# Kernel optimization log

Measured on AMD Instinct MI355X. Metric: run time of the kernel, lower is better.

## Reference

```python
import jax, jax.numpy as jnp
import numpy as np

N, T, D_MODEL, H, DK = 4, 4096, 1024, 16, 64


def setup_inputs() -> dict:
    key = jax.random.key(0)
    ks = jax.random.split(key, 16)
    randn = lambda k, sh: jax.random.normal(k, sh, dtype=jnp.float32)
    # linear weights stored (in, out) so y = x @ W + b (math-equivalent to torch Linear)
    scale = 1.0 / np.sqrt(D_MODEL)
    return {
        "x_k": randn(ks[0], (N, T, D_MODEL)),
        "x_v": randn(ks[1], (N, T, D_MODEL)),
        "x_q": randn(ks[2], (N, T, D_MODEL)),
        "mask": jnp.ones((N, T), dtype=jnp.int32),
        "Wk": randn(ks[3], (D_MODEL, H * DK)) * scale,
        "bk": randn(ks[4], (H * DK,)) * 0.02,
        "Wv": randn(ks[5], (D_MODEL, H * DK)) * scale,
        "bv": randn(ks[6], (H * DK,)) * 0.02,
        "Wq": randn(ks[7], (D_MODEL, H * DK)) * scale,
        "bq": randn(ks[8], (H * DK,)) * 0.02,
        "alpha_w": randn(ks[9], (DK,)),
        "beta_w": randn(ks[10], (DK,)),
        "Wr": randn(ks[11], (DK, DK)) * (1.0 / np.sqrt(DK)),
        "br": randn(ks[12], (DK,)) * 0.02,
        "Wfc": randn(ks[13], (H * DK, D_MODEL)) * scale,
        "bfc": randn(ks[14], (D_MODEL,)) * 0.02,
    }


def _split_heads(x):  # (n, t, h*d) -> (n, h, t, d)
    n, t, _ = x.shape
    return x.reshape(n, t, H, DK).transpose(0, 2, 1, 3)


def reference(x_k, x_v, x_q, mask, Wk, bk, Wv, bv, Wq, bq,
              alpha_w, beta_w, Wr, br, Wfc, bfc):
    scale = DK ** (-0.5)
    k = _split_heads(x_k @ Wk + bk)  # (n, h, t, d)
    v = _split_heads(x_v @ Wv + bv)
    q = _split_heads(x_q @ Wq + bq)

    m = (mask == 0)[:, None, :]  # (n, 1, t) True where masked
    neg_inf = jnp.finfo(q.dtype).min

    # alpha pooling over queries -> global query (n, h, d)
    alpha = jnp.einsum('nhtd,d->nht', q, alpha_w) * scale
    alpha = jnp.where(m, neg_inf, alpha)
    alpha = jax.nn.softmax(alpha, axis=-1)
    global_query = jnp.einsum('nht,nhtd->nhd', alpha, q)

    # p = broadcast(global_query) * k, then beta pooling -> global key
    p = global_query[:, :, None, :] * k  # (n, h, t, d)
    beta = jnp.einsum('nhtd,d->nht', p, beta_w) * scale
    beta = jnp.where(m, neg_inf, beta)
    beta = jax.nn.softmax(beta, axis=-1)
    global_key = jnp.einsum('nht,nhtd->nhd', beta, p)

    u = global_key[:, :, None, :] * v  # (n, h, t, d)
    u_r = u @ Wr + br
    A = u_r + q  # (n, h, t, d)
    A = A.transpose(0, 2, 1, 3).reshape(N, T, H * DK)
    return A @ Wfc + bfc
```

## Files before the change

kernel.cpp:

```cpp
#include <hip/hip_runtime.h>

typedef __bf16 bf16x8 __attribute__((ext_vector_type(8)));
typedef float f32x4 __attribute__((ext_vector_type(4)));
typedef unsigned int u32x4 __attribute__((ext_vector_type(4)));
typedef unsigned short u16x4 __attribute__((ext_vector_type(4)));
typedef unsigned short u16x8 __attribute__((ext_vector_type(8)));

#define SEQ_T 4096
#define DMODEL 1024
#define HEADS 16
#define DKH 64
#define MTOK 16384

#define AS1 __attribute__((address_space(1)))
#define AS3 __attribute__((address_space(3)))

__device__ __forceinline__ unsigned short f2bf(float f) {
  unsigned u = __builtin_bit_cast(unsigned int, f);
  u += 0x7FFFu + ((u >> 16) & 1u);
  return (unsigned short)(u >> 16);
}
__device__ __forceinline__ float bf2f(unsigned short h) {
  unsigned u = ((unsigned)h) << 16;
  return __builtin_bit_cast(float, u);
}
__device__ __forceinline__ void gload16(const unsigned short* g, unsigned short* l) {
  __builtin_amdgcn_global_load_lds((const AS1 unsigned int*)(g),
                                   (AS3 unsigned int*)(l), 16, 0, 0);
}

__global__ void __launch_bounds__(256) k_cvt(const float* __restrict__ x,
                                             unsigned short* __restrict__ y,
                                             long long nelem) {
  long long i = ((long long)blockIdx.x * 256 + threadIdx.x) * 8;
  if (i >= nelem) return;
  u16x8 o;
#pragma unroll
  for (int j = 0; j < 8; ++j) o[j] = f2bf(x[i + j]);
  *(u16x8*)(y + i) = o;
}

__global__ void __launch_bounds__(256) k_wtrans(const float* __restrict__ W,
                                                unsigned short* __restrict__ Wt,
                                                int K, int N) {
  __shared__ float tile[32][33];
  int bn = blockIdx.x * 32, bk = blockIdx.y * 32;
  int tx = threadIdx.x, ty = threadIdx.y;
#pragma unroll
  for (int j = 0; j < 32; j += 8)
    tile[ty + j][tx] = W[(size_t)(bk + ty + j) * N + bn + tx];
  __syncthreads();
#pragma unroll
  for (int j = 0; j < 32; j += 8)
    Wt[(size_t)(bn + ty + j) * K + bk + tx] = f2bf(tile[tx][ty + j]);
}

#define BM 128
#define BN 128
#define BK 32

template <int OBF, int SCORE>
__global__ void __launch_bounds__(256, 2)
k_gemm(const unsigned short* __restrict__ A, const unsigned short* __restrict__ Bt,
       const float* __restrict__ bias, void* __restrict__ C,
       const int* __restrict__ mask, const float* __restrict__ swt,
       float* __restrict__ sbuf, int M, int N, int K) {
  __shared__ unsigned short As[BM * BK];
  __shared__ unsigned short Bs[BN * BK];
  const int tid = threadIdx.x;
  const int lane = tid & 63, wid = tid >> 6;
  const int wr = wid >> 1, wc = wid & 1;
  const int bnb = blockIdx.x;
  const int bm = blockIdx.y * BM, bn = bnb * BN;
  const int l15 = lane & 15, l4 = lane >> 4;

  f32x4 acc[4][4];
#pragma unroll
  for (int i = 0; i < 4; ++i)
#pragma unroll
    for (int j = 0; j < 4; ++j)
#pragma unroll
      for (int e = 0; e < 4; ++e) acc[i][j][e] = 0.f;

  const int srow = wid * 32 + (lane >> 2);
  const int scol = (lane & 3) * 8;
  const unsigned short* Ag = A + (size_t)(bm + srow) * K + scol;
  const unsigned short* Bg = Bt + (size_t)(bn + srow) * K + scol;
  unsigned short* Al = As + wid * 32 * BK;
  unsigned short* Bl = Bs + wid * 32 * BK;

  for (int kt = 0; kt < K; kt += BK) {
    __syncthreads();
    gload16(Ag + kt, Al);
    gload16(Ag + kt + 16 * K, Al + 16 * BK);
    gload16(Bg + kt, Bl);
    gload16(Bg + kt + 16 * K, Bl + 16 * BK);
    __syncthreads();
    bf16x8 af[4], bfr[4];
#pragma unroll
    for (int m = 0; m < 4; ++m)
      af[m] = *(const bf16x8*)(As + (wr * 64 + m * 16 + l15) * BK + l4 * 8);
#pragma unroll
    for (int n = 0; n < 4; ++n)
      bfr[n] = *(const bf16x8*)(Bs + (wc * 64 + n * 16 + l15) * BK + l4 * 8);
#pragma unroll
    for (int m = 0; m < 4; ++m)
#pragma unroll
      for (int n = 0; n < 4; ++n)
        acc[m][n] = __builtin_amdgcn_mfma_f32_16x16x32_bf16(af[m], bfr[n],
                                                            acc[m][n], 0, 0, 0);
  }

  const int crow = bm + wr * 64 + l4 * 4;
  const int ccol = bn + wc * 64 + l15;

  float pacc[4][4];
  const float* wrow = nullptr;
  if (SCORE == 1) wrow = swt;
  if (SCORE == 2) wrow = swt + ((size_t)((bm >> 12) * HEADS + bnb * 2 + wc)) * DKH;
  if (SCORE) {
#pragma unroll
    for (int m = 0; m < 4; ++m)
#pragma unroll
      for (int e = 0; e < 4; ++e) pacc[m][e] = 0.f;
  }

#pragma unroll
  for (int m = 0; m < 4; ++m)
#pragma unroll
    for (int n = 0; n < 4; ++n) {
      int c = ccol + n * 16;
      float bj = bias[c];
      float wg = SCORE ? wrow[n * 16 + l15] : 0.f;
#pragma unroll
      for (int e = 0; e < 4; ++e) {
        int r = crow + m * 16 + e;
        float v = acc[m][n][e] + bj;
        if (SCORE) pacc[m][e] += v * wg;
        if (OBF)
          ((unsigned short*)C)[(size_t)r * N + c] = f2bf(v);
        else
          ((float*)C)[(size_t)r * N + c] = v;
      }
    }

  if (SCORE) {
#pragma unroll
    for (int m = 0; m < 4; ++m)
#pragma unroll
      for (int e = 0; e < 4; ++e) {
        float p = pacc[m][e];
        p += __shfl_xor(p, 1);
        p += __shfl_xor(p, 2);
        p += __shfl_xor(p, 4);
        p += __shfl_xor(p, 8);
        if (l15 == 0) {
          int r = crow + m * 16 + e;
          int t = r & (SEQ_T - 1), n = r >> 12;
          float sc = p * 0.125f;
          if (mask[n * SEQ_T + t] == 0) sc = -3.0e38f;
          sbuf[((size_t)n * HEADS + bnb * 2 + wc) * SEQ_T + t] = sc;
        }
      }
  }
}

__global__ void __launch_bounds__(256) k_stat1(const float* __restrict__ s,
                                               float* __restrict__ pmax,
                                               float* __restrict__ psum) {
  __shared__ float red[4];
  const int b = blockIdx.x, tid = threadIdx.x, lane = tid & 63, wid = tid >> 6;
  float v = s[(size_t)b * 256 + tid];
  float m = v;
#pragma unroll
  for (int o = 1; o < 64; o <<= 1) m = fmaxf(m, __shfl_xor(m, o));
  if (lane == 0) red[wid] = m;
  __syncthreads();
  m = fmaxf(fmaxf(red[0], red[1]), fmaxf(red[2], red[3]));
  __syncthreads();
  float e = __expf(v - m);
#pragma unroll
  for (int o = 1; o < 64; o <<= 1) e += __shfl_xor(e, o);
  if (lane == 0) red[wid] = e;
  __syncthreads();
  if (tid == 0) {
    pmax[b] = m;
    psum[b] = red[0] + red[1] + red[2] + red[3];
  }
}

__global__ void __launch_bounds__(64) k_stat2(const float* __restrict__ pmax,
                                              const float* __restrict__ psum,
                                              float* __restrict__ smx,
                                              float* __restrict__ sinv) {
  const int b = blockIdx.x, lane = threadIdx.x;
  float pm = -3.4e38f, ps = 0.f;
  if (lane < 16) {
    pm = pmax[b * 16 + lane];
    ps = psum[b * 16 + lane];
  }
  float gm = pm;
#pragma unroll
  for (int o = 1; o < 16; o <<= 1) gm = fmaxf(gm, __shfl_xor(gm, o));
  float sc = ps * __expf(pm - gm);
#pragma unroll
  for (int o = 1; o < 16; o <<= 1) sc += __shfl_xor(sc, o);
  if (lane == 0) {
    smx[b] = gm;
    sinv[b] = 1.f / sc;
  }
}

__global__ void __launch_bounds__(256) k_wsum(const unsigned short* __restrict__ X,
                                              const float* __restrict__ s,
                                              const float* __restrict__ mxv,
                                              const float* __restrict__ invv,
                                              float* __restrict__ pbuf) {
  __shared__ float part[16][64];
  const int nh = blockIdx.x >> 4, chunk = blockIdx.x & 15;
  const int n = nh >> 4, h = nh & 15;
  const int tid = threadIdx.x, lane = tid & 63, wid = tid >> 6;
  const int tsub = lane >> 4, dl = lane & 15;
  const float mx = mxv[nh], inv = invv[nh];
  const float* sb = s + (size_t)nh * SEQ_T + chunk * 256;
  const size_t base = ((size_t)n * SEQ_T + chunk * 256) * DMODEL + h * DKH + dl * 4;
  f32x4 acc = {0.f, 0.f, 0.f, 0.f};
  for (int t = wid * 4 + tsub; t < 256; t += 16) {
    float w = __expf(sb[t] - mx) * inv;
    u16x4 xv = *(const u16x4*)(X + base + (size_t)t * DMODEL);
    acc[0] += w * bf2f(xv[0]);
    acc[1] += w * bf2f(xv[1]);
    acc[2] += w * bf2f(xv[2]);
    acc[3] += w * bf2f(xv[3]);
  }
  int g = wid * 4 + tsub;
#pragma unroll
  for (int e = 0; e < 4; ++e) part[g][dl * 4 + e] = acc[e];
  __syncthreads();
  if (tid < 64) {
    float v = 0.f;
#pragma unroll
    for (int gg = 0; gg < 16; ++gg) v += part[gg][tid];
    pbuf[(size_t)blockIdx.x * 64 + tid] = v;
  }
}

template <int MODE>
__global__ void __launch_bounds__(64) k_fin(const float* __restrict__ pbuf,
                                            const float* __restrict__ gq,
                                            const float* __restrict__ bw,
                                            float* __restrict__ out,
                                            float* __restrict__ wv) {
  const int nh = blockIdx.x, d = threadIdx.x;
  float v = 0.f;
#pragma unroll
  for (int c = 0; c < 16; ++c) v += pbuf[((size_t)nh * 16 + c) * 64 + d];
  if (MODE == 1) v *= gq[(size_t)nh * 64 + d];
  out[(size_t)nh * 64 + d] = v;
  if (MODE == 0) wv[(size_t)nh * 64 + d] = v * bw[d];
}

__global__ void __launch_bounds__(256) k_wrg(const float* __restrict__ gk,
                                             const float* __restrict__ Wr,
                                             unsigned short* __restrict__ WrgT) {
  const int nh = blockIdx.x, tid = threadIdx.x;
#pragma unroll
  for (int i = 0; i < 16; ++i) {
    int idx = i * 256 + tid;
    int d = idx >> 6, dd = idx & 63;
    WrgT[(size_t)nh * 4096 + idx] = f2bf(gk[nh * 64 + dd] * Wr[dd * 64 + d]);
  }
}

#define ABM 128
#define VLD 72
__global__ void __launch_bounds__(256) k_abuild2(const unsigned short* __restrict__ v,
                                                 const unsigned short* __restrict__ qbf,
                                                 const unsigned short* __restrict__ WrgT,
                                                 const float* __restrict__ br,
                                                 unsigned short* __restrict__ A) {
  __shared__ unsigned short Vs[ABM * VLD];
  __shared__ unsigned short Ws[DKH * VLD];
  const int tid = threadIdx.x, lane = tid & 63, wid = tid >> 6;
  const int nh = blockIdx.y;
  const int n = nh >> 4, h = nh & 15;
  const size_t nt0 = (size_t)n * SEQ_T + (size_t)blockIdx.x * ABM;
  const size_t vbase = nt0 * DMODEL + (size_t)h * DKH;
#pragma unroll
  for (int p = 0; p < 4; ++p) {
    int idx = p * 256 + tid;
    int row = idx >> 3, c = idx & 7;
    *(u32x4*)(Vs + row * VLD + c * 8) =
        *(const u32x4*)(v + vbase + (size_t)row * DMODEL + c * 8);
  }
#pragma unroll
  for (int p = 0; p < 2; ++p) {
    int idx = p * 256 + tid;
    int row = idx >> 3, c = idx & 7;
    *(u32x4*)(Ws + row * VLD + c * 8) =
        *(const u32x4*)(WrgT + (size_t)nh * 4096 + row * 64 + c * 8);
  }
  __syncthreads();
  const int l15 = lane & 15, l4 = lane >> 4;
  f32x4 acc[2][4];
#pragma unroll
  for (int m = 0; m < 2; ++m)
#pragma unroll
    for (int nf = 0; nf < 4; ++nf)
#pragma unroll
      for (int e = 0; e < 4; ++e) acc[m][nf][e] = 0.f;
#pragma unroll
  for (int ks = 0; ks < 2; ++ks) {
    bf16x8 af[2], bfr[4];
#pragma unroll
    for (int m = 0; m < 2; ++m)
      af[m] = *(const bf16x8*)(Vs + (wid * 32 + m * 16 + l15) * VLD + l4 * 8 + ks * 32);
#pragma unroll
    for (int nf = 0; nf < 4; ++nf)
      bfr[nf] = *(const bf16x8*)(Ws + (nf * 16 + l15) * VLD + l4 * 8 + ks * 32);
#pragma unroll
    for (int m = 0; m < 2; ++m)
#pragma unroll
      for (int nf = 0; nf < 4; ++nf)
        acc[m][nf] = __builtin_amdgcn_mfma_f32_16x16x32_bf16(af[m], bfr[nf],
                                                             acc[m][nf], 0, 0, 0);
  }
#pragma unroll
  for (int m = 0; m < 2; ++m)
#pragma unroll
    for (int nf = 0; nf < 4; ++nf) {
      int d = nf * 16 + l15;
      float bj = br[d];
#pragma unroll
      for (int e = 0; e < 4; ++e) {
        int r = wid * 32 + m * 16 + l4 * 4 + e;
        size_t off = vbase + (size_t)r * DMODEL + d;
        float val = acc[m][nf][e] + bj + bf2f(qbf[off]);
        A[off] = f2bf(val);
      }
    }
}

extern "C" void kernel_launch(void* const* d_in, const int* in_sizes, int n_in,
                              void* d_out, int out_size, void* d_ws, size_t ws_size,
                              hipStream_t stream) {
  const float* x_k = (const float*)d_in[0];
  const float* x_v = (const float*)d_in[1];
  const float* x_q = (const float*)d_in[2];
  const int* mask = (const int*)d_in[3];
  const float* Wk = (const float*)d_in[4];
  const float* bk = (const float*)d_in[5];
  const float* Wv = (const float*)d_in[6];
  const float* bv = (const float*)d_in[7];
  const float* Wq = (const float*)d_in[8];
  const float* bq = (const float*)d_in[9];
  const float* alpha_w = (const float*)d_in[10];
  const float* beta_w = (const float*)d_in[11];
  const float* Wr = (const float*)d_in[12];
  const float* br = (const float*)d_in[13];
  const float* Wfc = (const float*)d_in[14];
  const float* bfc = (const float*)d_in[15];

  unsigned short* qbf = (unsigned short*)d_out;

  char* ws = (char*)d_ws;
  const size_t SZ_XBF = (size_t)MTOK * DMODEL * 2;
  unsigned short* kbf = (unsigned short*)(ws);
  unsigned short* vbf = (unsigned short*)(ws + SZ_XBF);
  unsigned short* xst = (unsigned short*)(ws + 2 * SZ_XBF);
  unsigned short* WkT = (unsigned short*)(ws + 3 * SZ_XBF);
  unsigned short* WvT = WkT + (size_t)DMODEL * DMODEL;
  unsigned short* WqT = WvT + (size_t)DMODEL * DMODEL;
  unsigned short* WfT = WqT + (size_t)DMODEL * DMODEL;
  unsigned short* WrgT = WfT + (size_t)DMODEL * DMODEL;
  float* gq = (float*)(WrgT + (size_t)64 * 4096);
  float* gk = gq + 4096;
  float* wvb = gk + 4096;
  float* sbuf = wvb + 4096;
  float* pbuf = sbuf + (size_t)64 * SEQ_T;
  float* pmax = pbuf + 1024 * 64;
  float* psum = pmax + 1024;
  float* smx = psum + 1024;
  float* sinv = smx + 64;

  dim3 tb(32, 8);
  dim3 tg(DMODEL / 32, DMODEL / 32);
  k_wtrans<<<tg, tb, 0, stream>>>(Wq, WqT, DMODEL, DMODEL);
  k_wtrans<<<tg, tb, 0, stream>>>(Wk, WkT, DMODEL, DMODEL);
  k_wtrans<<<tg, tb, 0, stream>>>(Wv, WvT, DMODEL, DMODEL);
  k_wtrans<<<tg, tb, 0, stream>>>(Wfc, WfT, DMODEL, DMODEL);

  long long nx = (long long)MTOK * DMODEL;
  int cvtg = (int)(nx / 8 / 256);
  dim3 ggrid(DMODEL / BN, MTOK / BM);

  k_cvt<<<cvtg, 256, 0, stream>>>(x_q, xst, nx);
  k_gemm<1, 1><<<ggrid, 256, 0, stream>>>(xst, WqT, bq, (void*)qbf, mask, alpha_w,
                                          sbuf, MTOK, DMODEL, DMODEL);
  k_stat1<<<1024, 256, 0, stream>>>(sbuf, pmax, psum);
  k_stat2<<<64, 64, 0, stream>>>(pmax, psum, smx, sinv);
  k_wsum<<<1024, 256, 0, stream>>>(qbf, sbuf, smx, sinv, pbuf);
  k_fin<0><<<64, 64, 0, stream>>>(pbuf, nullptr, beta_w, gq, wvb);

  k_cvt<<<cvtg, 256, 0, stream>>>(x_k, xst, nx);
  k_gemm<1, 2><<<ggrid, 256, 0, stream>>>(xst, WkT, bk, (void*)kbf, mask, wvb,
                                          sbuf, MTOK, DMODEL, DMODEL);
  k_stat1<<<1024, 256, 0, stream>>>(sbuf, pmax, psum);
  k_stat2<<<64, 64, 0, stream>>>(pmax, psum, smx, sinv);
  k_wsum<<<1024, 256, 0, stream>>>(kbf, sbuf, smx, sinv, pbuf);
  k_fin<1><<<64, 64, 0, stream>>>(pbuf, gq, nullptr, gk, nullptr);

  k_cvt<<<cvtg, 256, 0, stream>>>(x_v, xst, nx);
  k_gemm<1, 0><<<ggrid, 256, 0, stream>>>(xst, WvT, bv, (void*)vbf, nullptr, nullptr,
                                          nullptr, MTOK, DMODEL, DMODEL);

  k_wrg<<<64, 256, 0, stream>>>(gk, Wr, WrgT);
  dim3 agrid(SEQ_T / ABM, 64);
  k_abuild2<<<agrid, 256, 0, stream>>>(vbf, qbf, WrgT, br, xst);

  k_gemm<0, 0><<<ggrid, 256, 0, stream>>>(xst, WfT, bfc, d_out, nullptr, nullptr,
                                          nullptr, MTOK, DMODEL, DMODEL);
}
```

Before: 328.4 us.

## Eliminate K projection GEMM and fold Wr/global key into V weights

The full K projection GEMM is replaced by algebra. Beta scores are computed as x_k times a per-batch folded weight (Wk·(gq⊙beta_w)), giving a narrow 16-column GEMM. The global key is obtained by pooling raw x_k with the softmax weights and then projecting through Wk. The V projection, the Wr mixing and the q residual are fused into a single GEMM with per-batch combined weights (Wv·diag(gk)·Wr) and a combined bias, which removes the separate abuild pass and the kbf/vbf intermediates. In exchange it adds several small weight-prep kernels, an fp32 pooled pass over x_k, and per-batch weight matrices that change the rounding behaviour.

Measured after the change: 320.5 us. 1.02x faster.

```diff
diff --git a/kernel.cpp b/kernel.cpp
--- a/kernel.cpp
+++ b/kernel.cpp
@@ -59,12 +59,13 @@
 #define BN 128
 #define BK 32
 
-template <int OBF, int SCORE>
+template <int OBF, int SCORE, int FUSEA>
 __global__ void __launch_bounds__(256, 2)
 k_gemm(const unsigned short* __restrict__ A, const unsigned short* __restrict__ Bt,
        const float* __restrict__ bias, void* __restrict__ C,
        const int* __restrict__ mask, const float* __restrict__ swt,
-       float* __restrict__ sbuf, int M, int N, int K) {
+       float* __restrict__ sbuf, const unsigned short* __restrict__ qadd,
+       int M, int N, int K) {
   __shared__ unsigned short As[BM * BK];
   __shared__ unsigned short Bs[BN * BK];
   const int tid = threadIdx.x;
@@ -74,6 +75,9 @@
   const int bm = blockIdx.y * BM, bn = bnb * BN;
   const int l15 = lane & 15, l4 = lane >> 4;
 
+  const unsigned short* Btn = FUSEA ? Bt + ((size_t)(bm >> 12) << 20) : Bt;
+  const float* biasn = FUSEA ? bias + ((bm >> 12) << 10) : bias;
+
   f32x4 acc[4][4];
 #pragma unroll
   for (int i = 0; i < 4; ++i)
@@ -85,7 +89,7 @@
   const int srow = wid * 32 + (lane >> 2);
   const int scol = (lane & 3) * 8;
   const unsigned short* Ag = A + (size_t)(bm + srow) * K + scol;
-  const unsigned short* Bg = Bt + (size_t)(bn + srow) * K + scol;
+  const unsigned short* Bg = Btn + (size_t)(bn + srow) * K + scol;
   unsigned short* Al = As + wid * 32 * BK;
   unsigned short* Bl = Bs + wid * 32 * BK;
 
@@ -117,7 +121,6 @@
   float pacc[4][4];
   const float* wrow = nullptr;
   if (SCORE == 1) wrow = swt;
-  if (SCORE == 2) wrow = swt + ((size_t)((bm >> 12) * HEADS + bnb * 2 + wc)) * DKH;
   if (SCORE) {
 #pragma unroll
     for (int m = 0; m < 4; ++m)
@@ -130,12 +133,13 @@
 #pragma unroll
     for (int n = 0; n < 4; ++n) {
       int c = ccol + n * 16;
-      float bj = bias[c];
+      float bj = biasn[c];
       float wg = SCORE ? wrow[n * 16 + l15] : 0.f;
 #pragma unroll
       for (int e = 0; e < 4; ++e) {
         int r = crow + m * 16 + e;
         float v = acc[m][n][e] + bj;
+        if (FUSEA) v += bf2f(qadd[(size_t)r * N + c]);
         if (SCORE) pacc[m][e] += v * wg;
         if (OBF)
           ((unsigned short*)C)[(size_t)r * N + c] = f2bf(v);
@@ -245,9 +249,7 @@
   }
 }
 
-template <int MODE>
 __global__ void __launch_bounds__(64) k_fin(const float* __restrict__ pbuf,
-                                            const float* __restrict__ gq,
                                             const float* __restrict__ bw,
                                             float* __restrict__ out,
                                             float* __restrict__ wv) {
@@ -255,9 +257,167 @@
   float v = 0.f;
 #pragma unroll
   for (int c = 0; c < 16; ++c) v += pbuf[((size_t)nh * 16 + c) * 64 + d];
-  if (MODE == 1) v *= gq[(size_t)nh * 64 + d];
   out[(size_t)nh * 64 + d] = v;
-  if (MODE == 0) wv[(size_t)nh * 64 + d] = v * bw[d];
+  wv[(size_t)nh * 64 + d] = v * bw[d];
+}
+
+__global__ void __launch_bounds__(256) k_wks(const float* __restrict__ Wk,
+                                             const float* __restrict__ wv,
+                                             unsigned short* __restrict__ WksT) {
+  const int nh = blockIdx.x, tid = threadIdx.x;
+  const int n = nh >> 4, h = nh & 15;
+  __shared__ float wvs[64];
+  if (tid < 64) wvs[tid] = wv[(size_t)nh * 64 + tid];
+  __syncthreads();
+  int c0 = tid * 4;
+  u16x4 o;
+#pragma unroll
+  for (int i = 0; i < 4; ++i) {
+    int c = c0 + i;
+    const float* wr = Wk + (size_t)c * DMODEL + h * DKH;
+    float acc = 0.f;
+#pragma unroll
+    for (int dd = 0; dd < 64; dd += 4) {
+      f32x4 w4 = *(const f32x4*)(wr + dd);
+      acc += w4[0] * wvs[dd] + w4[1] * wvs[dd + 1] + w4[2] * wvs[dd + 2] +
+             w4[3] * wvs[dd + 3];
+    }
+    o[i] = f2bf(acc);
+  }
+  *(u16x4*)(WksT + (size_t)n * 16 * DMODEL + (size_t)h * DMODEL + c0) = o;
+}
+
+__global__ void __launch_bounds__(64) k_bks(const float* __restrict__ bk,
+                                            const float* __restrict__ wv,
+                                            float* __restrict__ bks) {
+  const int nh = blockIdx.x, dd = threadIdx.x;
+  const int h = nh & 15;
+  float p = bk[h * 64 + dd] * wv[(size_t)nh * 64 + dd];
+#pragma unroll
+  for (int o = 1; o < 64; o <<= 1) p += __shfl_xor(p, o);
+  if (dd == 0) bks[nh] = p;
+}
+
+__global__ void __launch_bounds__(128) k_score(const unsigned short* __restrict__ xk,
+                                               const unsigned short* __restrict__ WksT,
+                                               const float* __restrict__ bks,
+                                               const int* __restrict__ mask,
+                                               float* __restrict__ sbuf) {
+  __shared__ unsigned short Xs[64 * 32];
+  __shared__ unsigned short Ws[16 * 32];
+  const int tid = threadIdx.x, lane = tid & 63, wid = tid >> 6;
+  const int l15 = lane & 15, l4 = lane >> 4;
+  const int bm = blockIdx.x * 64;
+  const int n = bm >> 12;
+  const unsigned short* Wn = WksT + (size_t)n * 16 * DMODEL;
+
+  f32x4 acc[2];
+#pragma unroll
+  for (int m = 0; m < 2; ++m)
+#pragma unroll
+    for (int e = 0; e < 4; ++e) acc[m][e] = 0.f;
+
+  const int srow = lane >> 2, scol = (lane & 3) * 8;
+  for (int kt = 0; kt < DMODEL; kt += 32) {
+    __syncthreads();
+#pragma unroll
+    for (int j = 0; j < 2; ++j) {
+      int rb = wid * 32 + j * 16;
+      gload16(xk + (size_t)(bm + rb + srow) * DMODEL + kt + scol, Xs + rb * 32);
+    }
+    if (wid == 0) gload16(Wn + (size_t)srow * DMODEL + kt + scol, Ws);
+    __syncthreads();
+    bf16x8 bfr = *(const bf16x8*)(Ws + l15 * 32 + l4 * 8);
+#pragma unroll
+    for (int m = 0; m < 2; ++m) {
+      bf16x8 af = *(const bf16x8*)(Xs + (wid * 32 + m * 16 + l15) * 32 + l4 * 8);
+      acc[m] = __builtin_amdgcn_mfma_f32_16x16x32_bf16(af, bfr, acc[m], 0, 0, 0);
+    }
+  }
+  const int h = l15;
+  const float bh = bks[n * 16 + h];
+#pragma unroll
+  for (int m = 0; m < 2; ++m)
+#pragma unroll
+    for (int e = 0; e < 4; ++e) {
+      int r = bm + wid * 32 + m * 16 + l4 * 4 + e;
+      int t = r & (SEQ_T - 1);
+      float sc = (acc[m][e] + bh) * 0.125f;
+      if (mask[n * SEQ_T + t] == 0) sc = -3.0e38f;
+      sbuf[((size_t)n * HEADS + h) * SEQ_T + t] = sc;
+    }
+}
+
+__global__ void __launch_bounds__(256) k_bwsum(const float* __restrict__ xk,
+                                               const float* __restrict__ s,
+                                               const float* __restrict__ smx,
+                                               const float* __restrict__ sinv,
+                                               float* __restrict__ part) {
+  __shared__ float eb[16][64];
+  const int tc = blockIdx.x, n = blockIdx.y, tid = threadIdx.x;
+#pragma unroll
+  for (int i = 0; i < 4; ++i) {
+    int idx = i * 256 + tid;
+    int h = idx >> 6, t = idx & 63;
+    int nh = n * 16 + h;
+    eb[h][t] = __expf(s[(size_t)nh * SEQ_T + tc * 64 + t] - smx[nh]) * sinv[nh];
+  }
+  __syncthreads();
+  const int c0 = tid * 4;
+  f32x4 acc[16];
+#pragma unroll
+  for (int h = 0; h < 16; ++h)
+#pragma unroll
+    for (int e = 0; e < 4; ++e) acc[h][e] = 0.f;
+  const float* xb = xk + ((size_t)n * SEQ_T + tc * 64) * DMODEL + c0;
+  for (int t = 0; t < 64; ++t) {
+    f32x4 x = *(const f32x4*)(xb + (size_t)t * DMODEL);
+#pragma unroll
+    for (int h = 0; h < 16; ++h) {
+      float w = eb[h][t];
+      acc[h][0] += w * x[0];
+      acc[h][1] += w * x[1];
+      acc[h][2] += w * x[2];
+      acc[h][3] += w * x[3];
+    }
+  }
+#pragma unroll
+  for (int h = 0; h < 16; ++h)
+    *(f32x4*)(part + (((size_t)(n * 64 + tc)) * 16 + h) * DMODEL + c0) = acc[h];
+}
+
+__global__ void __launch_bounds__(256) k_bred(const float* __restrict__ part,
+                                              float* __restrict__ pooled) {
+  const int nh = blockIdx.x, tid = threadIdx.x;
+  const int n = nh >> 4, h = nh & 15;
+  const int c0 = tid * 4;
+  f32x4 acc = {0.f, 0.f, 0.f, 0.f};
+  for (int tc = 0; tc < 64; ++tc) {
+    f32x4 p = *(const f32x4*)(part + (((size_t)(n * 64 + tc)) * 16 + h) * DMODEL + c0);
+    acc[0] += p[0]; acc[1] += p[1]; acc[2] += p[2]; acc[3] += p[3];
+  }
+  *(f32x4*)(pooled + (size_t)nh * DMODEL + c0) = acc;
+}
+
+__global__ void __launch_bounds__(64) k_gk(const float* __restrict__ pooled,
+                                           const unsigned short* __restrict__ WkT,
+                                           const float* __restrict__ bk,
+                                           const float* __restrict__ gq,
+                                           float* __restrict__ gk) {
+  __shared__ float pl[DMODEL];
+  const int nh = blockIdx.x, dd = threadIdx.x;
+  const int h = nh & 15;
+#pragma unroll
+  for (int i = 0; i < 16; ++i) pl[i * 64 + dd] = pooled[(size_t)nh * DMODEL + i * 64 + dd];
+  __syncthreads();
+  const unsigned short* wr = WkT + (size_t)(h * 64 + dd) * DMODEL;
+  float acc = 0.f;
+  for (int c = 0; c < DMODEL; c += 8) {
+    u16x8 w = *(const u16x8*)(wr + c);
+#pragma unroll
+    for (int j = 0; j < 8; ++j) acc += pl[c + j] * bf2f(w[j]);
+  }
+  gk[(size_t)nh * 64 + dd] = gq[(size_t)nh * 64 + dd] * (acc + bk[h * 64 + dd]);
 }
 
 __global__ void __launch_bounds__(256) k_wrg(const float* __restrict__ gk,
@@ -272,73 +432,67 @@
   }
 }
 
-#define ABM 128
-#define VLD 72
-__global__ void __launch_bounds__(256) k_abuild2(const unsigned short* __restrict__ v,
-                                                 const unsigned short* __restrict__ qbf,
-                                                 const unsigned short* __restrict__ WrgT,
-                                                 const float* __restrict__ br,
-                                                 unsigned short* __restrict__ A) {
-  __shared__ unsigned short Vs[ABM * VLD];
-  __shared__ unsigned short Ws[DKH * VLD];
+#define LDW 72
+__global__ void __launch_bounds__(256) k_wcomb(const unsigned short* __restrict__ WrgT,
+                                               const unsigned short* __restrict__ WvN,
+                                               unsigned short* __restrict__ WcombT) {
+  __shared__ unsigned short Wg[64 * LDW];
+  __shared__ unsigned short Vv[128 * LDW];
+  const int rc = blockIdx.x, nh = blockIdx.y;
+  const int n = nh >> 4, h = nh & 15;
   const int tid = threadIdx.x, lane = tid & 63, wid = tid >> 6;
-  const int nh = blockIdx.y;
+  const int l15 = lane & 15, l4 = lane >> 4;
+#pragma unroll
+  for (int i = 0; i < 2; ++i) {
+    int v = i * 256 + tid;
+    int d = v >> 3, k8 = v & 7;
+    *(u16x8*)(Wg + d * LDW + k8 * 8) =
+        *(const u16x8*)(WrgT + (size_t)nh * 4096 + d * 64 + k8 * 8);
+  }
+#pragma unroll
+  for (int i = 0; i < 4; ++i) {
+    int v = i * 256 + tid;
+    int r = v >> 3, k8 = v & 7;
+    *(u16x8*)(Vv + r * LDW + k8 * 8) =
+        *(const u16x8*)(WvN + (size_t)(rc * 128 + r) * DMODEL + h * 64 + k8 * 8);
+  }
+  __syncthreads();
+  f32x4 acc[8];
+#pragma unroll
+  for (int ct = 0; ct < 8; ++ct)
+#pragma unroll
+    for (int e = 0; e < 4; ++e) acc[ct][e] = 0.f;
+#pragma unroll
+  for (int ks = 0; ks < 2; ++ks) {
+    bf16x8 af = *(const bf16x8*)(Wg + (wid * 16 + l15) * LDW + ks * 32 + l4 * 8);
+#pragma unroll
+    for (int ct = 0; ct < 8; ++ct) {
+      bf16x8 bf = *(const bf16x8*)(Vv + (ct * 16 + l15) * LDW + ks * 32 + l4 * 8);
+      acc[ct] = __builtin_amdgcn_mfma_f32_16x16x32_bf16(af, bf, acc[ct], 0, 0, 0);
+    }
+  }
+  unsigned short* out = WcombT + ((size_t)n << 20);
+#pragma unroll
+  for (int ct = 0; ct < 8; ++ct)
+#pragma unroll
+    for (int e = 0; e < 4; ++e) {
+      int d = h * 64 + wid * 16 + l4 * 4 + e;
+      int r = rc * 128 + ct * 16 + l15;
+      out[(size_t)d * DMODEL + r] = f2bf(acc[ct][e]);
+    }
+}
+
+__global__ void __launch_bounds__(64) k_bcomb(const float* __restrict__ bv,
+                                              const unsigned short* __restrict__ WrgT,
+                                              const float* __restrict__ br,
+                                              float* __restrict__ bcomb) {
+  const int nh = blockIdx.x, d = threadIdx.x;
   const int n = nh >> 4, h = nh & 15;
-  const size_t nt0 = (size_t)n * SEQ_T + (size_t)blockIdx.x * ABM;
-  const size_t vbase = nt0 * DMODEL + (size_t)h * DKH;
-#pragma unroll
-  for (int p = 0; p < 4; ++p) {
-    int idx = p * 256 + tid;
-    int row = idx >> 3, c = idx & 7;
-    *(u32x4*)(Vs + row * VLD + c * 8) =
-        *(const u32x4*)(v + vbase + (size_t)row * DMODEL + c * 8);
-  }
-#pragma unroll
-  for (int p = 0; p < 2; ++p) {
-    int idx = p * 256 + tid;
-    int row = idx >> 3, c = idx & 7;
-    *(u32x4*)(Ws + row * VLD + c * 8) =
-        *(const u32x4*)(WrgT + (size_t)nh * 4096 + row * 64 + c * 8);
-  }
-  __syncthreads();
-  const int l15 = lane & 15, l4 = lane >> 4;
-  f32x4 acc[2][4];
-#pragma unroll
-  for (int m = 0; m < 2; ++m)
-#pragma unroll
-    for (int nf = 0; nf < 4; ++nf)
-#pragma unroll
-      for (int e = 0; e < 4; ++e) acc[m][nf][e] = 0.f;
-#pragma unroll
-  for (int ks = 0; ks < 2; ++ks) {
-    bf16x8 af[2], bfr[4];
-#pragma unroll
-    for (int m = 0; m < 2; ++m)
-      af[m] = *(const bf16x8*)(Vs + (wid * 32 + m * 16 + l15) * VLD + l4 * 8 + ks * 32);
-#pragma unroll
-    for (int nf = 0; nf < 4; ++nf)
-      bfr[nf] = *(const bf16x8*)(Ws + (nf * 16 + l15) * VLD + l4 * 8 + ks * 32);
-#pragma unroll
-    for (int m = 0; m < 2; ++m)
-#pragma unroll
-      for (int nf = 0; nf < 4; ++nf)
-        acc[m][nf] = __builtin_amdgcn_mfma_f32_16x16x32_bf16(af[m], bfr[nf],
-                                                             acc[m][nf], 0, 0, 0);
-  }
-#pragma unroll
-  for (int m = 0; m < 2; ++m)
-#pragma unroll
-    for (int nf = 0; nf < 4; ++nf) {
-      int d = nf * 16 + l15;
-      float bj = br[d];
-#pragma unroll
-      for (int e = 0; e < 4; ++e) {
-        int r = wid * 32 + m * 16 + l4 * 4 + e;
-        size_t off = vbase + (size_t)r * DMODEL + d;
-        float val = acc[m][nf][e] + bj + bf2f(qbf[off]);
-        A[off] = f2bf(val);
-      }
-    }
+  float acc = br[d];
+#pragma unroll
+  for (int dd = 0; dd < 64; ++dd)
+    acc += bv[h * 64 + dd] * bf2f(WrgT[(size_t)nh * 4096 + d * 64 + dd]);
+  bcomb[(size_t)n * DMODEL + h * 64 + d] = acc;
 }
 
 extern "C" void kernel_launch(void* const* d_in, const int* in_sizes, int n_in,
@@ -364,60 +518,72 @@
   unsigned short* qbf = (unsigned short*)d_out;
 
   char* ws = (char*)d_ws;
-  const size_t SZ_XBF = (size_t)MTOK * DMODEL * 2;
-  unsigned short* kbf = (unsigned short*)(ws);
-  unsigned short* vbf = (unsigned short*)(ws + SZ_XBF);
-  unsigned short* xst = (unsigned short*)(ws + 2 * SZ_XBF);
-  unsigned short* WkT = (unsigned short*)(ws + 3 * SZ_XBF);
-  unsigned short* WvT = WkT + (size_t)DMODEL * DMODEL;
-  unsigned short* WqT = WvT + (size_t)DMODEL * DMODEL;
-  unsigned short* WfT = WqT + (size_t)DMODEL * DMODEL;
-  unsigned short* WrgT = WfT + (size_t)DMODEL * DMODEL;
-  float* gq = (float*)(WrgT + (size_t)64 * 4096);
-  float* gk = gq + 4096;
-  float* wvb = gk + 4096;
-  float* sbuf = wvb + 4096;
+  const size_t MB = 1024 * 1024;
+  unsigned short* xst = (unsigned short*)(ws);
+  unsigned short* abuf = (unsigned short*)(ws + 32 * MB);
+  unsigned short* WqT = (unsigned short*)(ws + 64 * MB);
+  unsigned short* WkT = WqT + (size_t)DMODEL * DMODEL;
+  unsigned short* WfT = WkT + (size_t)DMODEL * DMODEL;
+  unsigned short* WvN = WfT + (size_t)DMODEL * DMODEL;
+  unsigned short* WcombT = WvN + (size_t)DMODEL * DMODEL;
+  unsigned short* WrgT = WcombT + (size_t)4 * DMODEL * DMODEL;
+  unsigned short* WksT = WrgT + (size_t)64 * 4096;
+  float* part = (float*)(WksT + (size_t)4 * 16 * DMODEL);
+  float* pooled = part + (size_t)256 * 16 * DMODEL;
+  float* sbuf = pooled + (size_t)64 * DMODEL;
   float* pbuf = sbuf + (size_t)64 * SEQ_T;
   float* pmax = pbuf + 1024 * 64;
   float* psum = pmax + 1024;
   float* smx = psum + 1024;
   float* sinv = smx + 64;
+  float* gq = sinv + 64;
+  float* wvb = gq + 4096;
+  float* gk = wvb + 4096;
+  float* bks = gk + 4096;
+  float* bcomb = bks + 64;
 
   dim3 tb(32, 8);
   dim3 tg(DMODEL / 32, DMODEL / 32);
   k_wtrans<<<tg, tb, 0, stream>>>(Wq, WqT, DMODEL, DMODEL);
   k_wtrans<<<tg, tb, 0, stream>>>(Wk, WkT, DMODEL, DMODEL);
-  k_wtrans<<<tg, tb, 0, stream>>>(Wv, WvT, DMODEL, DMODEL);
   k_wtrans<<<tg, tb, 0, stream>>>(Wfc, WfT, DMODEL, DMODEL);
+  k_cvt<<<512, 256, 0, stream>>>(Wv, WvN, (long long)DMODEL * DMODEL);
 
   long long nx = (long long)MTOK * DMODEL;
   int cvtg = (int)(nx / 8 / 256);
   dim3 ggrid(DMODEL / BN, MTOK / BM);
 
   k_cvt<<<cvtg, 256, 0, stream>>>(x_q, xst, nx);
-  k_gemm<1, 1><<<ggrid, 256, 0, stream>>>(xst, WqT, bq, (void*)qbf, mask, alpha_w,
-                                          sbuf, MTOK, DMODEL, DMODEL);
+  k_gemm<1, 1, 0><<<ggrid, 256, 0, stream>>>(xst, WqT, bq, (void*)qbf, mask,
+                                             alpha_w, sbuf, nullptr,
+                                             MTOK, DMODEL, DMODEL);
   k_stat1<<<1024, 256, 0, stream>>>(sbuf, pmax, psum);
   k_stat2<<<64, 64, 0, stream>>>(pmax, psum, smx, sinv);
   k_wsum<<<1024, 256, 0, stream>>>(qbf, sbuf, smx, sinv, pbuf);
-  k_fin<0><<<64, 64, 0, stream>>>(pbuf, nullptr, beta_w, gq, wvb);
-
+  k_fin<<<64, 64, 0, stream>>>(pbuf, beta_w, gq, wvb);
+
+  k_wks<<<64, 256, 0, stream>>>(Wk, wvb, WksT);
+  k_bks<<<64, 64, 0, stream>>>(bk, wvb, bks);
   k_cvt<<<cvtg, 256, 0, stream>>>(x_k, xst, nx);
-  k_gemm<1, 2><<<ggrid, 256, 0, stream>>>(xst, WkT, bk, (void*)kbf, mask, wvb,
-                                          sbuf, MTOK, DMODEL, DMODEL);
+  k_score<<<MTOK / 64, 128, 0, stream>>>(xst, WksT, bks, mask, sbuf);
   k_stat1<<<1024, 256, 0, stream>>>(sbuf, pmax, psum);
   k_stat2<<<64, 64, 0, stream>>>(pmax, psum, smx, sinv);
-  k_wsum<<<1024, 256, 0, stream>>>(kbf, sbuf, smx, sinv, pbuf);
-  k_fin<1><<<64, 64, 0, stream>>>(pbuf, gq, nullptr, gk, nullptr);
+  dim3 bwg(64, 4);
+  k_bwsum<<<bwg, 256, 0, stream>>>(x_k, sbuf, smx, sinv, part);
+  k_bred<<<64, 256, 0, stream>>>(part, pooled);
+  k_gk<<<64, 64, 0, stream>>>(pooled, WkT, bk, gq, gk);
+
+  k_wrg<<<64, 256, 0, stream>>>(gk, Wr, WrgT);
+  dim3 wcg(8, 64);
+  k_wcomb<<<wcg, 256, 0, stream>>>(WrgT, WvN, WcombT);
+  k_bcomb<<<64, 64, 0, stream>>>(bv, WrgT, br, bcomb);
 
   k_cvt<<<cvtg, 256, 0, stream>>>(x_v, xst, nx);
-  k_gemm<1, 0><<<ggrid, 256, 0, stream>>>(xst, WvT, bv, (void*)vbf, nullptr, nullptr,
-                                          nullptr, MTOK, DMODEL, DMODEL);
-
-  k_wrg<<<64, 256, 0, stream>>>(gk, Wr, WrgT);
-  dim3 agrid(SEQ_T / ABM, 64);
-  k_abuild2<<<agrid, 256, 0, stream>>>(vbf, qbf, WrgT, br, xst);
-
-  k_gemm<0, 0><<<ggrid, 256, 0, stream>>>(xst, WfT, bfc, d_out, nullptr, nullptr,
-                                          nullptr, MTOK, DMODEL, DMODEL);
-}
+  k_gemm<1, 0, 1><<<ggrid, 256, 0, stream>>>(xst, WcombT, bcomb, (void*)abuf,
+                                             nullptr, nullptr, nullptr, qbf,
+                                             MTOK, DMODEL, DMODEL);
+
+  k_gemm<0, 0, 0><<<ggrid, 256, 0, stream>>>(abuf, WfT, bfc, d_out, nullptr,
+                                             nullptr, nullptr, nullptr,
+                                             MTOK, DMODEL, DMODEL);
+}
```
